# Kernel tuning notes

Measured on AMD Instinct MI355X. Metric: run time of the kernel, lower is better.

## Reference

```python
import jax, jax.numpy as jnp
import numpy as np

N, C_IN, H, W = 32, 16, 256, 256
C_OUT, K = 64, 3

def setup_inputs() -> dict:
    key = jax.random.key(0)
    kx, kw, kb = jax.random.split(key, 3)
    x = jax.random.normal(kx, (N, C_IN, H, W), dtype=jnp.float32)
    # PyTorch Conv2d default init: U(-b, b), b = 1/sqrt(fan_in)
    bound = 1.0 / np.sqrt(C_IN * K * K)
    conv_weight = jax.random.uniform(kw, (C_OUT, C_IN, K, K), minval=-bound, maxval=bound, dtype=jnp.float32)
    conv_bias = jax.random.uniform(kb, (C_OUT,), minval=-bound, maxval=bound, dtype=jnp.float32)
    return {"x": x, "conv_weight": conv_weight, "conv_bias": conv_bias}

def reference(x, conv_weight, conv_bias):
    # conv2d, stride=1, padding=0 (VALID), NCHW / OIHW
    y = jax.lax.conv_general_dilated(
        x, conv_weight,
        window_strides=(1, 1), padding="VALID",
        dimension_numbers=("NCHW", "OIHW", "NCHW"))
    y = y + conv_bias[None, :, None, None]
    # min over output channels (keepdim -> 1 channel), then double tanh
    y = jnp.min(y, axis=1, keepdims=True)  # [N,1,OH,OW]
    return jnp.tanh(jnp.tanh(y))
```

## Files before the change

### kernel.cpp

```cpp
#include <hip/hip_runtime.h>

typedef __bf16 bf16x8 __attribute__((ext_vector_type(8)));
typedef unsigned short us8 __attribute__((ext_vector_type(8)));
typedef float f32x16 __attribute__((ext_vector_type(16)));

#define N_IMG 32
#define CI 16
#define HH 256
#define WW 256
#define CO 64
#define OHH 254
#define OWW 254

#define XS_W 258
#define XS_C 24
#define WS_K 168

__device__ __forceinline__ unsigned short f2bf(float f) {
  union { float f; unsigned u; } v; v.f = f;
  return (unsigned short)((v.u + 0x7FFFu + ((v.u >> 16) & 1u)) >> 16);
}

__device__ __forceinline__ float fast_tanh(float x) {
  float cx = fminf(fmaxf(x, -15.f), 15.f);
  float e = __expf(2.f * cx);
  return (e - 1.f) / (e + 1.f);
}

__global__ __launch_bounds__(256, 2)
void conv_min_tanh(const float* __restrict__ xg, const float* __restrict__ wg,
                   const float* __restrict__ bg, float* __restrict__ out) {
  __shared__ __align__(16) unsigned short xs[3 * XS_W * XS_C];
  __shared__ __align__(16) unsigned short ws[CO * WS_K];

  const int t = threadIdx.x;
  const int n = blockIdx.x / OHH;
  const int oh = blockIdx.x % OHH;

#pragma unroll
  for (int i = 0; i < 36; ++i) {
    int f = i * 256 + t;
    int oc = f / 144;
    int r = f - oc * 144;
    int ci = r / 9;
    int tap = r - ci * 9;
    ws[oc * WS_K + tap * 16 + ci] = f2bf(wg[f]);
  }
  if (t < CO) ws[t * WS_K + 144] = f2bf(bg[t]);
  for (int i = t; i < CO * 15; i += 256) {
    int oc = i / 15;
    ws[oc * WS_K + 145 + (i - oc * 15)] = 0;
  }

  {
    const size_t base_n = (size_t)n * CI * HH * WW;
#pragma unroll
    for (int kh = 0; kh < 3; ++kh) {
#pragma unroll
      for (int half = 0; half < 2; ++half) {
        float v[8];
#pragma unroll
        for (int j = 0; j < 8; ++j) {
          int ci = half * 8 + j;
          v[j] = xg[base_n + ((size_t)ci * HH + (oh + kh)) * WW + t];
        }
        us8 pk;
#pragma unroll
        for (int j = 0; j < 8; ++j) pk[j] = f2bf(v[j]);
        *(us8*)(xs + (kh * XS_W + t) * XS_C + half * 8) = pk;
      }
    }
  }
  if (t < 96) {
    int kh = t >> 5;
    int rem = t & 31;
    int w = 256 + (rem >> 4);
    int ci = rem & 15;
    xs[(kh * XS_W + w) * XS_C + ci] = 0;
  }
  __syncthreads();

  const int lane = t & 63;
  const int wave = t >> 6;
  const int lr = lane & 31;
  const int qh = lane >> 5;

  bf16x8 afrag[2][10];
#pragma unroll
  for (int mt = 0; mt < 2; ++mt) {
    const unsigned short* wp = ws + (mt * 32 + lr) * WS_K + qh * 8;
#pragma unroll
    for (int tap = 0; tap < 10; ++tap)
      afrag[mt][tap] = __builtin_bit_cast(bf16x8, *(const us8*)(wp + tap * 16));
  }

  f32x16 acc[2][2];
#pragma unroll
  for (int a = 0; a < 2; ++a)
#pragma unroll
    for (int b = 0; b < 2; ++b)
#pragma unroll
      for (int e = 0; e < 16; ++e) acc[a][b][e] = 0.f;

  const unsigned short* xp = xs + (wave * 64 + lr) * XS_C + qh * 8;

#pragma unroll
  for (int tap = 0; tap < 9; ++tap) {
    const int kh = tap / 3, kw = tap - kh * 3;
#pragma unroll
    for (int nt = 0; nt < 2; ++nt) {
      bf16x8 xf = __builtin_bit_cast(
          bf16x8, *(const us8*)(xp + (kh * XS_W + nt * 32 + kw) * XS_C));
      acc[0][nt] = __builtin_amdgcn_mfma_f32_32x32x16_bf16(afrag[0][tap], xf,
                                                           acc[0][nt], 0, 0, 0);
      acc[1][nt] = __builtin_amdgcn_mfma_f32_32x32x16_bf16(afrag[1][tap], xf,
                                                           acc[1][nt], 0, 0, 0);
    }
  }
  {
    us8 one = {};
    if (qh == 0) one[0] = 0x3F80;
    bf16x8 xone = __builtin_bit_cast(bf16x8, one);
#pragma unroll
    for (int nt = 0; nt < 2; ++nt) {
      acc[0][nt] = __builtin_amdgcn_mfma_f32_32x32x16_bf16(afrag[0][9], xone,
                                                           acc[0][nt], 0, 0, 0);
      acc[1][nt] = __builtin_amdgcn_mfma_f32_32x32x16_bf16(afrag[1][9], xone,
                                                           acc[1][nt], 0, 0, 0);
    }
  }

  float vmin[2];
#pragma unroll
  for (int nt = 0; nt < 2; ++nt) {
    float v = acc[0][nt][0];
#pragma unroll
    for (int e = 1; e < 16; ++e) v = fminf(v, acc[0][nt][e]);
#pragma unroll
    for (int e = 0; e < 16; ++e) v = fminf(v, acc[1][nt][e]);
    v = fminf(v, __shfl_xor(v, 32, 64));
    vmin[nt] = fast_tanh(fast_tanh(v));
  }
  float res = (lane < 32) ? vmin[0] : vmin[1];
  int ow = wave * 64 + lane;
  if (ow < OWW) out[((size_t)n * OHH + oh) * OWW + ow] = res;
}

extern "C" void kernel_launch(void* const* d_in, const int* in_sizes, int n_in,
                              void* d_out, int out_size, void* d_ws, size_t ws_size,
                              hipStream_t stream) {
  const float* x = (const float*)d_in[0];
  const float* w = (const float*)d_in[1];
  const float* b = (const float*)d_in[2];
  float* out = (float*)d_out;
  conv_min_tanh<<<dim3(N_IMG * OHH), dim3(256), 0, stream>>>(x, w, b, out);
}
```

Measured before the change: 255.8 us.

## Pre-convert input to channel-last bf16 in workspace and drop per-block LDS staging

```diff
diff --git a/kernel.cpp b/kernel.cpp
--- a/kernel.cpp
+++ b/kernel.cpp
@@ -12,9 +12,10 @@
 #define OHH 254
 #define OWW 254
 
-#define XS_W 258
-#define XS_C 24
-#define WS_K 168
+#define WP_SHORTS (CO * 160)
+#define XP_OFF_SHORTS 16384
+#define XP_SHORTS ((size_t)N_IMG * HH * WW * CI)
+#define WS_NEEDED ((XP_OFF_SHORTS + XP_SHORTS) * 2)
 
 __device__ __forceinline__ unsigned short f2bf(float f) {
   union { float f; unsigned u; } v; v.f = f;
@@ -26,17 +27,112 @@
   float e = __expf(2.f * cx);
   return (e - 1.f) / (e + 1.f);
 }
+
+__global__ void prep_w(const float* __restrict__ wg, const float* __restrict__ bg,
+                       unsigned short* __restrict__ wp) {
+  int idx = blockIdx.x * 256 + threadIdx.x;
+  if (idx >= WP_SHORTS) return;
+  int oc = idx / 160;
+  int k = idx - oc * 160;
+  int tap = k >> 4, ci = k & 15;
+  float v;
+  if (tap < 9)      v = wg[oc * 144 + ci * 9 + tap];
+  else if (ci == 0) v = bg[oc];
+  else              v = 0.f;
+  wp[idx] = f2bf(v);
+}
+
+__global__ void prep_x(const float* __restrict__ xg, unsigned short* __restrict__ xp) {
+  const int bi = blockIdx.x;
+  const int t = threadIdx.x;
+  const int n = bi >> 8, h = bi & 255;
+  const float* src = xg + (size_t)n * (CI * HH * WW) + (size_t)h * WW + t;
+  us8 a, b;
+#pragma unroll
+  for (int ci = 0; ci < 8; ++ci) a[ci] = f2bf(src[(size_t)ci * (HH * WW)]);
+#pragma unroll
+  for (int ci = 0; ci < 8; ++ci) b[ci] = f2bf(src[(size_t)(ci + 8) * (HH * WW)]);
+  unsigned short* dst = xp + ((size_t)bi * WW + t) * CI;
+  *(us8*)dst = a;
+  *(us8*)(dst + 8) = b;
+}
+
+__global__ __launch_bounds__(256, 4)
+void conv_main(const unsigned short* __restrict__ wp,
+               const unsigned short* __restrict__ xp, float* __restrict__ out) {
+  const int t = threadIdx.x;
+  const int n = blockIdx.x / OHH;
+  const int oh = blockIdx.x % OHH;
+  const int lane = t & 63, wave = t >> 6;
+  const int lr = lane & 31, qh = lane >> 5;
+
+  const unsigned short* xb = xp + ((size_t)n * HH + oh) * (WW * CI) + qh * 8;
+  const unsigned short* wpl = wp + lr * 160 + qh * 8;
+  const int p = wave * 64 + lr;
+
+  f32x16 acc[2][2];
+#pragma unroll
+  for (int a = 0; a < 2; ++a)
+#pragma unroll
+    for (int b = 0; b < 2; ++b)
+#pragma unroll
+      for (int e = 0; e < 16; ++e) acc[a][b][e] = 0.f;
+
+#pragma unroll
+  for (int tap = 0; tap < 9; ++tap) {
+    const int kh = tap / 3, kw = tap - kh * 3;
+    bf16x8 af0 = __builtin_bit_cast(bf16x8, *(const us8*)(wpl + tap * 16));
+    bf16x8 af1 = __builtin_bit_cast(bf16x8, *(const us8*)(wpl + 32 * 160 + tap * 16));
+#pragma unroll
+    for (int nt = 0; nt < 2; ++nt) {
+      int w = p + nt * 32 + kw;
+      w = (w > 255) ? 255 : w;
+      bf16x8 xf = __builtin_bit_cast(bf16x8, *(const us8*)(xb + kh * (WW * CI) + w * CI));
+      acc[0][nt] = __builtin_amdgcn_mfma_f32_32x32x16_bf16(af0, xf, acc[0][nt], 0, 0, 0);
+      acc[1][nt] = __builtin_amdgcn_mfma_f32_32x32x16_bf16(af1, xf, acc[1][nt], 0, 0, 0);
+    }
+  }
+  {
+    us8 one = {};
+    if (qh == 0) one[0] = 0x3F80;
+    bf16x8 xone = __builtin_bit_cast(bf16x8, one);
+    bf16x8 af0 = __builtin_bit_cast(bf16x8, *(const us8*)(wpl + 9 * 16));
+    bf16x8 af1 = __builtin_bit_cast(bf16x8, *(const us8*)(wpl + 32 * 160 + 9 * 16));
+#pragma unroll
+    for (int nt = 0; nt < 2; ++nt) {
+      acc[0][nt] = __builtin_amdgcn_mfma_f32_32x32x16_bf16(af0, xone, acc[0][nt], 0, 0, 0);
+      acc[1][nt] = __builtin_amdgcn_mfma_f32_32x32x16_bf16(af1, xone, acc[1][nt], 0, 0, 0);
+    }
+  }
+
+  float vmin[2];
+#pragma unroll
+  for (int nt = 0; nt < 2; ++nt) {
+    float v = acc[0][nt][0];
+#pragma unroll
+    for (int e = 1; e < 16; ++e) v = fminf(v, acc[0][nt][e]);
+#pragma unroll
+    for (int e = 0; e < 16; ++e) v = fminf(v, acc[1][nt][e]);
+    v = fminf(v, __shfl_xor(v, 32, 64));
+    vmin[nt] = fast_tanh(fast_tanh(v));
+  }
+  float res = (lane < 32) ? vmin[0] : vmin[1];
+  int ow = wave * 64 + lane;
+  if (ow < OWW) out[((size_t)n * OHH + oh) * OWW + ow] = res;
+}
+
+#define XS_W 258
+#define XS_C 24
+#define WS_K 168
 
 __global__ __launch_bounds__(256, 2)
 void conv_min_tanh(const float* __restrict__ xg, const float* __restrict__ wg,
                    const float* __restrict__ bg, float* __restrict__ out) {
   __shared__ __align__(16) unsigned short xs[3 * XS_W * XS_C];
   __shared__ __align__(16) unsigned short ws[CO * WS_K];
-
   const int t = threadIdx.x;
   const int n = blockIdx.x / OHH;
   const int oh = blockIdx.x % OHH;
-
 #pragma unroll
   for (int i = 0; i < 36; ++i) {
     int f = i * 256 + t;
@@ -51,7 +147,6 @@
     int oc = i / 15;
     ws[oc * WS_K + 145 + (i - oc * 15)] = 0;
   }
-
   {
     const size_t base_n = (size_t)n * CI * HH * WW;
 #pragma unroll
@@ -79,21 +174,16 @@
     xs[(kh * XS_W + w) * XS_C + ci] = 0;
   }
   __syncthreads();
-
-  const int lane = t & 63;
-  const int wave = t >> 6;
-  const int lr = lane & 31;
-  const int qh = lane >> 5;
-
+  const int lane = t & 63, wave = t >> 6;
+  const int lr = lane & 31, qh = lane >> 5;
   bf16x8 afrag[2][10];
 #pragma unroll
   for (int mt = 0; mt < 2; ++mt) {
-    const unsigned short* wp = ws + (mt * 32 + lr) * WS_K + qh * 8;
+    const unsigned short* wq = ws + (mt * 32 + lr) * WS_K + qh * 8;
 #pragma unroll
     for (int tap = 0; tap < 10; ++tap)
-      afrag[mt][tap] = __builtin_bit_cast(bf16x8, *(const us8*)(wp + tap * 16));
-  }
-
+      afrag[mt][tap] = __builtin_bit_cast(bf16x8, *(const us8*)(wq + tap * 16));
+  }
   f32x16 acc[2][2];
 #pragma unroll
   for (int a = 0; a < 2; ++a)
@@ -101,16 +191,14 @@
     for (int b = 0; b < 2; ++b)
 #pragma unroll
       for (int e = 0; e < 16; ++e) acc[a][b][e] = 0.f;
-
-  const unsigned short* xp = xs + (wave * 64 + lr) * XS_C + qh * 8;
-
+  const unsigned short* xq = xs + (wave * 64 + lr) * XS_C + qh * 8;
 #pragma unroll
   for (int tap = 0; tap < 9; ++tap) {
     const int kh = tap / 3, kw = tap - kh * 3;
 #pragma unroll
     for (int nt = 0; nt < 2; ++nt) {
       bf16x8 xf = __builtin_bit_cast(
-          bf16x8, *(const us8*)(xp + (kh * XS_W + nt * 32 + kw) * XS_C));
+          bf16x8, *(const us8*)(xq + (kh * XS_W + nt * 32 + kw) * XS_C));
       acc[0][nt] = __builtin_amdgcn_mfma_f32_32x32x16_bf16(afrag[0][tap], xf,
                                                            acc[0][nt], 0, 0, 0);
       acc[1][nt] = __builtin_amdgcn_mfma_f32_32x32x16_bf16(afrag[1][tap], xf,
@@ -129,7 +217,6 @@
                                                            acc[1][nt], 0, 0, 0);
     }
   }
-
   float vmin[2];
 #pragma unroll
   for (int nt = 0; nt < 2; ++nt) {
@@ -153,5 +240,13 @@
   const float* w = (const float*)d_in[1];
   const float* b = (const float*)d_in[2];
   float* out = (float*)d_out;
-  conv_min_tanh<<<dim3(N_IMG * OHH), dim3(256), 0, stream>>>(x, w, b, out);
-}
+  if (ws_size >= WS_NEEDED) {
+    unsigned short* wp = (unsigned short*)d_ws;
+    unsigned short* xpb = wp + XP_OFF_SHORTS;
+    prep_w<<<dim3((WP_SHORTS + 255) / 256), dim3(256), 0, stream>>>(w, b, wp);
+    prep_x<<<dim3(N_IMG * HH), dim3(256), 0, stream>>>(x, xpb);
+    conv_main<<<dim3(N_IMG * OHH), dim3(256), 0, stream>>>(wp, xpb, out);
+  } else {
+    conv_min_tanh<<<dim3(N_IMG * OHH), dim3(256), 0, stream>>>(x, w, b, out);
+  }
+}
```

After: 262.9 us. +2.8%, slower.
